# Optimization experiments

Hardware: AMD Instinct MI355X
Metric: run time of the kernel (lower is better)

Reference implementation:

```python
import jax, jax.numpy as jnp
import numpy as np

B, T, C = 8, 4096, 1024


def setup_inputs() -> dict:
    key = jax.random.key(0)
    ks = jax.random.split(key, 5)
    scales = (jnp.arange(C, dtype=jnp.float32) / C).reshape(1, 1, C)
    return {
        "x": jax.random.normal(ks[0], (B, T, C), dtype=jnp.float32),
        "time_decay": scales,
        "time_first": scales,
        "time_mix_k": scales,
        "time_mix_v": scales,
        "time_mix_r": scales,
        "Wk": jax.random.normal(ks[1], (C, C), dtype=jnp.float32) / np.sqrt(C),
        "Wv": jax.random.normal(ks[2], (C, C), dtype=jnp.float32) / np.sqrt(C),
        "Wr": jax.random.normal(ks[3], (C, C), dtype=jnp.float32) / np.sqrt(C),
        "Wo": jax.random.normal(ks[4], (C, C), dtype=jnp.float32) / np.sqrt(C),
    }


def _wkv(w_decay, u_first, k, v):
    # w_decay, u_first: [C]; k, v: [B, T, C]
    w = -jnp.exp(w_decay)  # per original: w = -w.exp()
    u = u_first
    kt = jnp.transpose(k, (1, 0, 2))  # [T, B, C]
    vt = jnp.transpose(v, (1, 0, 2))
    a0 = jnp.zeros((k.shape[0], k.shape[2]), dtype=k.dtype)
    b0 = jnp.zeros_like(a0)
    p0 = jnp.full_like(a0, -1e38)  # running max exponent

    def step(carry, kv):
        a, b, p = carry
        k_t, v_t = kv
        # output at t (includes bonus u for current token)
        q = jnp.maximum(p, u + k_t)
        e1 = jnp.exp(p - q)
        e2 = jnp.exp(u + k_t - q)
        y = (e1 * a + e2 * v_t) / (e1 * b + e2)
        # state update with decay w
        q2 = jnp.maximum(p + w, k_t)
        f1 = jnp.exp(p + w - q2)
        f2 = jnp.exp(k_t - q2)
        return (f1 * a + f2 * v_t, f1 * b + f2, q2), y

    _, y = jax.lax.scan(step, (a0, b0, p0), (kt, vt))
    return jnp.transpose(y, (1, 0, 2))  # [B, T, C]


def reference(x, time_decay, time_first, time_mix_k, time_mix_v, time_mix_r, Wk, Wv, Wr, Wo):
    # time shift: prev token, zero-padded at t=0 (ZeroPad2d((0,0,1,-1)))
    x_prev = jnp.pad(x, ((0, 0), (1, 0), (0, 0)))[:, :-1]
    # torch.lerp(a, b, w) = a + w*(b-a)
    xk = x_prev + time_mix_k * (x - x_prev)
    xv = x_prev + time_mix_v * (x - x_prev)
    xr = x_prev + time_mix_r * (x - x_prev)
    k = jnp.einsum('btc,dc->btd', xk, Wk)
    v = jnp.einsum('btc,dc->btd', xv, Wv)
    sr = jax.nn.sigmoid(jnp.einsum('btc,dc->btd', xr, Wr))
    wkv = _wkv(time_decay.reshape(-1), time_first.reshape(-1), k, v)
    return jnp.einsum('btc,dc->btd', sr * wkv, Wo)
```

## Files before the change

### kernel.cpp

```cpp
#include <hip/hip_runtime.h>
#include <hip/hip_bf16.h>
#include <hip/hip_fp16.h>


#define BH 8
#define TT 4096
#define CC 1024
#define NCH 64
#define CHL (TT / NCH)

typedef _Float16       f16x8  __attribute__((ext_vector_type(8)));
typedef float          f32x4  __attribute__((ext_vector_type(4)));
typedef unsigned short ushort_t;

__device__ __forceinline__ ushort_t f2h_u(float f) {
  return __half_as_ushort(__float2half(f));
}

#define GLOAD_LDS16(g, l)                                                     \
  __builtin_amdgcn_global_load_lds(                                           \
      (const __attribute__((address_space(1))) unsigned int*)(g),             \
      (__attribute__((address_space(3))) unsigned int*)(l), 16, 0, 0)

#define BARRIER() do { asm volatile("" ::: "memory");                        \
                       __builtin_amdgcn_s_barrier();                          \
                       asm volatile("" ::: "memory"); } while (0)

#define WAITALL() do { asm volatile("s_waitcnt vmcnt(0) lgkmcnt(0)" ::: "memory"); \
                       __builtin_amdgcn_sched_barrier(0); } while (0)

#define WAITV(n) do { asm volatile("s_waitcnt vmcnt(" #n ")" ::: "memory");  \
                      __builtin_amdgcn_sched_barrier(0); } while (0)

__global__ __launch_bounds__(256)
void split_w(const float* __restrict__ W0, const float* __restrict__ W1,
             const float* __restrict__ W2, const float* __restrict__ W3,
             ushort_t* __restrict__ out)
{
  int idx = blockIdx.x * 256 + threadIdx.x;
  int w = idx >> 20;
  int e = idx & (CC * CC - 1);
  const float* src = (w == 0) ? W0 : (w == 1) ? W1 : (w == 2) ? W2 : W3;
  out[(size_t)w * CC * CC + e] = f2h_u(src[e]);
}

__global__ __launch_bounds__(256)
void lerp3(const float* __restrict__ x,
           const float* __restrict__ mk, const float* __restrict__ mv,
           const float* __restrict__ mr,
           ushort_t* __restrict__ xk, ushort_t* __restrict__ xv,
           ushort_t* __restrict__ xr)
{
  const int idx = blockIdx.x * 256 + threadIdx.x;
  const int m = idx >> 8;
  const int c = (idx & 255) * 4;
  const size_t e = (size_t)m * CC + c;
  float4 cu = *(const float4*)(x + e);
  float4 pv = make_float4(0.f, 0.f, 0.f, 0.f);
  if ((m & (TT - 1)) != 0) pv = *(const float4*)(x + e - CC);

  const float* mixes[3] = {mk, mv, mr};
  ushort_t* outs[3] = {xk, xv, xr};
  #pragma unroll
  for (int z = 0; z < 3; ++z) {
    float4 mx = *(const float4*)(mixes[z] + c);
    float a0 = pv.x + mx.x * (cu.x - pv.x);
    float a1 = pv.y + mx.y * (cu.y - pv.y);
    float a2 = pv.z + mx.z * (cu.z - pv.z);
    float a3 = pv.w + mx.w * (cu.w - pv.w);
    *(ushort4*)(outs[z] + e) = make_ushort4(f2h_u(a0), f2h_u(a1), f2h_u(a2), f2h_u(a3));
  }
}

template<int EPI>
__global__ __launch_bounds__(512, 4)
void gemm_f16(const ushort_t* __restrict__ Ab, const ushort_t* __restrict__ Bb,
              void* __restrict__ Dv)
{
  constexpr int NS = 32;
  const size_t nbt = (size_t)BH * TT * CC;

  __shared__ __align__(16) ushort_t lds[2][12288];

  const int tid  = threadIdx.x;
  const int wave = tid >> 6, lane = tid & 63;
  const int wm = wave & 1, wn = wave >> 1;
  const int lr = lane & 15, kg = lane >> 4;

  const int z = blockIdx.z;
  const ushort_t* Ah = Ab + (size_t)z * nbt;
  const ushort_t* Bh = Bb + (size_t)z * CC * CC;

  const int bid = blockIdx.x;
  const int swz = (bid & 7) * 128 + (bid >> 3);
  const int m0 = (swz >> 2) * 128;
  const int n0 = (swz & 3) * 256;

  f32x4 acc[4][4] = {};

  auto stage = [&](int s) {
    if (s >= NS) return;
    const int kk = s * 32;
    {
      const int row = tid >> 2;
      const int q   = (tid & 3) ^ ((row >> 1) & 3);
      const ushort_t* src = Ah + (size_t)(m0 + row) * CC + kk + q * 8;
      ushort_t* dst = &lds[s & 1][0] + wave * 512;
      GLOAD_LDS16(src, dst);
    }
    #pragma unroll
    for (int c = 0; c < 2; ++c) {
      const int row = c * 128 + (tid >> 2);
      const int q   = (tid & 3) ^ ((row >> 1) & 3);
      const ushort_t* src = Bh + (size_t)(n0 + row) * CC + kk + q * 8;
      ushort_t* dst = &lds[s & 1][4096] + c * 4096 + wave * 512;
      GLOAD_LDS16(src, dst);
    }
  };
  auto rdA = [&](int b, int fm) -> f16x8 {
    const int row = wm * 64 + fm * 16 + lr;
    const int q   = kg ^ ((row >> 1) & 3);
    return *(const f16x8*)&lds[b][row * 32 + q * 8];
  };
  auto rdB = [&](int b, int fn) -> f16x8 {
    const int row = wn * 64 + fn * 16 + lr;
    const int q   = kg ^ ((row >> 1) & 3);
    return *(const f16x8*)&lds[b][4096 + row * 32 + q * 8];
  };

  stage(0); stage(1);
  WAITV(3);
  BARRIER();

  for (int s = 0; s < NS; ++s) {
    const int b = s & 1;

    f16x8 Bfr[4];
    #pragma unroll
    for (int fn = 0; fn < 4; ++fn) Bfr[fn] = rdB(b, fn);
    f16x8 Afr[4];
    #pragma unroll
    for (int fm = 0; fm < 4; ++fm) Afr[fm] = rdA(b, fm);

    __builtin_amdgcn_s_setprio(1);
    #pragma unroll
    for (int fm = 0; fm < 4; ++fm)
      #pragma unroll
      for (int fn = 0; fn < 4; ++fn)
        acc[fm][fn] = __builtin_amdgcn_mfma_f32_16x16x32_f16(Afr[fm], Bfr[fn], acc[fm][fn], 0, 0, 0);
    __builtin_amdgcn_s_setprio(0);

    WAITALL();
    BARRIER();
    stage(s + 2);
  }

  if (EPI == 0) {
    float* Df = (float*)Dv;
    #pragma unroll
    for (int fm = 0; fm < 4; ++fm)
      #pragma unroll
      for (int fn = 0; fn < 4; ++fn) {
        const int col  = n0 + wn * 64 + fn * 16 + lr;
        const int rowb = m0 + wm * 64 + fm * 16 + kg * 4;
        #pragma unroll
        for (int r = 0; r < 4; ++r)
          Df[(size_t)(rowb + r) * CC + col] = acc[fm][fn][r];
      }
  } else {
    __half* Dh = (__half*)Dv + (size_t)z * nbt;
    __half* ep = (__half*)&lds[0][0];
    const int rowl = tid >> 4;
    const int ck   = tid & 15;
    #pragma unroll
    for (int s = 0; s < 4; ++s) {
      __syncthreads();
      #pragma unroll
      for (int fn = 0; fn < 4; ++fn)
        #pragma unroll
        for (int r = 0; r < 4; ++r)
          ep[(wm * 16 + kg * 4 + r) * 280 + wn * 64 + fn * 16 + lr] =
              __float2half(acc[s][fn][r]);
      __syncthreads();
      uint4 v0 = *(const uint4*)&ep[rowl * 280 + ck * 16];
      uint4 v1 = *(const uint4*)&ep[rowl * 280 + ck * 16 + 8];
      const int grow = m0 + (rowl >> 4) * 64 + s * 16 + (rowl & 15);
      __half* dst = Dh + (size_t)grow * CC + n0 + ck * 16;
      *(uint4*)dst = v0;
      *(uint4*)(dst + 8) = v1;
    }
  }
}

__global__ __launch_bounds__(256)
void wkv_phase_a(const __half* __restrict__ kb, const __half* __restrict__ vb,
                 const float* __restrict__ decay,
                 float* __restrict__ SA, float* __restrict__ SB, float* __restrict__ SP)
{
  const int idx = blockIdx.x * 256 + threadIdx.x;
  const int c  = idx & (CC - 1);
  const int bc = idx >> 10;
  const int ch = bc & (NCH - 1);
  const int b  = bc >> 6;
  const float w = -__expf(decay[c]);
  float aa = 0.f, bb = 0.f, pp = -1e38f;
  size_t base = ((size_t)b * TT + (size_t)ch * CHL) * CC + c;
  #pragma unroll 4
  for (int t = 0; t < CHL; ++t) {
    const float kt = __half2float(kb[base]);
    const float vt = __half2float(vb[base]);
    const float q2 = fmaxf(pp + w, kt);
    const float f1 = __expf(pp + w - q2);
    const float f2 = __expf(kt - q2);
    aa = f1 * aa + f2 * vt; bb = f1 * bb + f2; pp = q2;
    base += CC;
  }
  SA[idx] = aa; SB[idx] = bb; SP[idx] = pp;
}

__global__ __launch_bounds__(256)
void wkv_combine(float* __restrict__ SA, float* __restrict__ SB, float* __restrict__ SP,
                 const float* __restrict__ decay)
{
  const int idx = blockIdx.x * 256 + threadIdx.x;
  const int c = idx & (CC - 1);
  const int b = idx >> 10;
  const float w  = -__expf(decay[c]);
  const float wL = w * (float)CHL;
  float aa = 0.f, bb = 0.f, pp = -1e38f;
  for (int ch = 0; ch < NCH; ++ch) {
    const size_t s = ((size_t)b * NCH + ch) * CC + c;
    const float la = SA[s], lb = SB[s], lp = SP[s];
    SA[s] = aa; SB[s] = bb; SP[s] = pp;
    const float pw = pp + wL;
    const float q  = fmaxf(pw, lp);
    const float e1 = __expf(pw - q);
    const float e2 = __expf(lp - q);
    aa = e1 * aa + e2 * la; bb = e1 * bb + e2 * lb; pp = q;
  }
}

__global__ __launch_bounds__(256)
void wkv_phase_c(const __half* __restrict__ kb, const __half* __restrict__ vb,
                 const __half* __restrict__ rb, const float* __restrict__ decay,
                 const float* __restrict__ first,
                 const float* __restrict__ SA, const float* __restrict__ SB,
                 const float* __restrict__ SP,
                 ushort_t* __restrict__ yh)
{
  const int idx = blockIdx.x * 256 + threadIdx.x;
  const int c  = idx & (CC - 1);
  const int bc = idx >> 10;
  const int ch = bc & (NCH - 1);
  const int b  = bc >> 6;
  const float w = -__expf(decay[c]);
  const float u = first[c];
  float aa = SA[idx], bb = SB[idx], pp = SP[idx];
  size_t base = ((size_t)b * TT + (size_t)ch * CHL) * CC + c;
  #pragma unroll 4
  for (int t = 0; t < CHL; ++t) {
    const float kt = __half2float(kb[base]);
    const float vt = __half2float(vb[base]);
    const float rt = __half2float(rb[base]);
    const float q  = fmaxf(pp, u + kt);
    const float e1 = __expf(pp - q);
    const float e2 = __expf(u + kt - q);
    const float yv = (e1 * aa + e2 * vt) / (e1 * bb + e2);
    const float sr = 1.f / (1.f + __expf(-rt));
    yh[base] = f2h_u(sr * yv);
    const float q2 = fmaxf(pp + w, kt);
    const float f1 = __expf(pp + w - q2);
    const float f2 = __expf(kt - q2);
    aa = f1 * aa + f2 * vt; bb = f1 * bb + f2; pp = q2;
    base += CC;
  }
}

extern "C" void kernel_launch(void* const* d_in, const int* in_sizes, int n_in,
                              void* d_out, int out_size, void* d_ws, size_t ws_size,
                              hipStream_t stream) {
  const float* x     = (const float*)d_in[0];
  const float* decay = (const float*)d_in[1];
  const float* first = (const float*)d_in[2];
  const float* mk    = (const float*)d_in[3];
  const float* mv    = (const float*)d_in[4];
  const float* mr    = (const float*)d_in[5];
  const float* Wk    = (const float*)d_in[6];
  const float* Wv    = (const float*)d_in[7];
  const float* Wr    = (const float*)d_in[8];
  const float* Wo    = (const float*)d_in[9];
  float* out = (float*)d_out;

  const size_t nbt = (size_t)BH * TT * CC;
  const size_t WS  = (size_t)CC * CC;
  char* p = (char*)d_ws;
  ushort_t* xk   = (ushort_t*)(p);
  ushort_t* xv   = (ushort_t*)(p +  67108864);
  ushort_t* xr   = (ushort_t*)(p + 134217728);
  __half*   kbuf = (__half*)  (p + 201326592);
  __half*   vbuf = (__half*)  (p + 268435456);
  __half*   rbuf = (__half*)  (p + 335544320);
  ushort_t* Wsp  = (ushort_t*)(p + 402653184);
  float*    SA   = (float*)   (p + 411041792);
  float*    SB   = (float*)   (p + 413138944);
  float*    SP   = (float*)   (p + 415236096);

  dim3 blk(256);
  const dim3 gblk(512);
  const unsigned lerpg = (unsigned)(nbt / 4 / 256);

  split_w<<<dim3(4 * CC * CC / 256), blk, 0, stream>>>(Wk, Wv, Wr, Wo, Wsp);
  lerp3<<<dim3(lerpg), blk, 0, stream>>>(x, mk, mv, mr, xk, xv, xr);

  gemm_f16<1><<<dim3(1024, 1, 3), gblk, 0, stream>>>(xk, Wsp, (void*)kbuf);

  const int nscan = BH * NCH * CC;
  wkv_phase_a<<<dim3(nscan / 256), blk, 0, stream>>>(kbuf, vbuf, decay, SA, SB, SP);
  wkv_combine<<<dim3(BH * CC / 256), blk, 0, stream>>>(SA, SB, SP, decay);
  wkv_phase_c<<<dim3(nscan / 256), blk, 0, stream>>>(kbuf, vbuf, rbuf, decay, first,
                                                     SA, SB, SP, xk);

  gemm_f16<0><<<dim3(1024, 1, 1), gblk, 0, stream>>>(xk, Wsp + 3 * WS, (void*)out);
}
```

Before: 517.4 us.

## Shrink GEMM tiles to 128x128 and load B fragments directly from global

```diff
diff --git a/kernel.cpp b/kernel.cpp
--- a/kernel.cpp
+++ b/kernel.cpp
@@ -73,14 +73,15 @@
 }
 
 template<int EPI>
-__global__ __launch_bounds__(512, 4)
+__global__ __launch_bounds__(256, 3)
 void gemm_f16(const ushort_t* __restrict__ Ab, const ushort_t* __restrict__ Bb,
               void* __restrict__ Dv)
 {
   constexpr int NS = 32;
   const size_t nbt = (size_t)BH * TT * CC;
 
-  __shared__ __align__(16) ushort_t lds[2][12288];
+  __shared__ __align__(16) ushort_t lds[2][4096];
+  __shared__ __align__(16) __half  ep[32 * 136];
 
   const int tid  = threadIdx.x;
   const int wave = tid >> 6, lane = tid & 63;
@@ -92,28 +93,22 @@
   const ushort_t* Bh = Bb + (size_t)z * CC * CC;
 
   const int bid = blockIdx.x;
-  const int swz = (bid & 7) * 128 + (bid >> 3);
-  const int m0 = (swz >> 2) * 128;
-  const int n0 = (swz & 3) * 256;
+  const int swz = (bid & 7) * 256 + (bid >> 3);
+  const int m0 = (swz >> 3) * 128;
+  const int n0 = (swz & 7) * 128;
 
   f32x4 acc[4][4] = {};
 
   auto stage = [&](int s) {
     if (s >= NS) return;
     const int kk = s * 32;
-    {
-      const int row = tid >> 2;
-      const int q   = (tid & 3) ^ ((row >> 1) & 3);
-      const ushort_t* src = Ah + (size_t)(m0 + row) * CC + kk + q * 8;
-      ushort_t* dst = &lds[s & 1][0] + wave * 512;
-      GLOAD_LDS16(src, dst);
-    }
     #pragma unroll
     for (int c = 0; c < 2; ++c) {
-      const int row = c * 128 + (tid >> 2);
-      const int q   = (tid & 3) ^ ((row >> 1) & 3);
-      const ushort_t* src = Bh + (size_t)(n0 + row) * CC + kk + q * 8;
-      ushort_t* dst = &lds[s & 1][4096] + c * 4096 + wave * 512;
+      const int slot = c * 256 + tid;
+      const int row  = slot >> 2;
+      const int q    = (slot & 3) ^ ((row >> 1) & 3);
+      const ushort_t* src = Ah + (size_t)(m0 + row) * CC + kk + q * 8;
+      ushort_t* dst = &lds[s & 1][0] + c * 2048 + wave * 512;
       GLOAD_LDS16(src, dst);
     }
   };
@@ -122,37 +117,59 @@
     const int q   = kg ^ ((row >> 1) & 3);
     return *(const f16x8*)&lds[b][row * 32 + q * 8];
   };
-  auto rdB = [&](int b, int fn) -> f16x8 {
-    const int row = wn * 64 + fn * 16 + lr;
-    const int q   = kg ^ ((row >> 1) & 3);
-    return *(const f16x8*)&lds[b][4096 + row * 32 + q * 8];
+  auto ldB = [&](int s, f16x8* Bf) {
+    const int kk = s * 32 + kg * 8;
+    #pragma unroll
+    for (int fn = 0; fn < 4; ++fn) {
+      const int row = n0 + wn * 64 + fn * 16 + lr;
+      Bf[fn] = *(const f16x8*)(Bh + (size_t)row * CC + kk);
+    }
   };
 
-  stage(0); stage(1);
-  WAITV(3);
+  f16x8 B0[4], B1[4];
+
+  stage(0);
+  ldB(0, B0);
+  stage(1);
+  WAITV(2);
   BARRIER();
 
-  for (int s = 0; s < NS; ++s) {
-    const int b = s & 1;
-
-    f16x8 Bfr[4];
-    #pragma unroll
-    for (int fn = 0; fn < 4; ++fn) Bfr[fn] = rdB(b, fn);
-    f16x8 Afr[4];
-    #pragma unroll
-    for (int fm = 0; fm < 4; ++fm) Afr[fm] = rdA(b, fm);
-
-    __builtin_amdgcn_s_setprio(1);
-    #pragma unroll
-    for (int fm = 0; fm < 4; ++fm)
-      #pragma unroll
-      for (int fn = 0; fn < 4; ++fn)
-        acc[fm][fn] = __builtin_amdgcn_mfma_f32_16x16x32_f16(Afr[fm], Bfr[fn], acc[fm][fn], 0, 0, 0);
-    __builtin_amdgcn_s_setprio(0);
-
-    WAITALL();
-    BARRIER();
-    stage(s + 2);
+  #pragma unroll 1
+  for (int t = 0; t < NS / 2; ++t) {
+    {
+      const int s = 2 * t;
+      f16x8 Afr[4];
+      #pragma unroll
+      for (int fm = 0; fm < 4; ++fm) Afr[fm] = rdA(0, fm);
+      ldB(s + 1, B1);
+      __builtin_amdgcn_s_setprio(1);
+      #pragma unroll
+      for (int fm = 0; fm < 4; ++fm)
+        #pragma unroll
+        for (int fn = 0; fn < 4; ++fn)
+          acc[fm][fn] = __builtin_amdgcn_mfma_f32_16x16x32_f16(Afr[fm], B0[fn], acc[fm][fn], 0, 0, 0);
+      __builtin_amdgcn_s_setprio(0);
+      WAITALL();
+      BARRIER();
+      stage(s + 2);
+    }
+    {
+      const int s = 2 * t + 1;
+      f16x8 Afr[4];
+      #pragma unroll
+      for (int fm = 0; fm < 4; ++fm) Afr[fm] = rdA(1, fm);
+      if (s + 1 < NS) ldB(s + 1, B0);
+      __builtin_amdgcn_s_setprio(1);
+      #pragma unroll
+      for (int fm = 0; fm < 4; ++fm)
+        #pragma unroll
+        for (int fn = 0; fn < 4; ++fn)
+          acc[fm][fn] = __builtin_amdgcn_mfma_f32_16x16x32_f16(Afr[fm], B1[fn], acc[fm][fn], 0, 0, 0);
+      __builtin_amdgcn_s_setprio(0);
+      WAITALL();
+      BARRIER();
+      stage(s + 2);
+    }
   }
 
   if (EPI == 0) {
@@ -169,9 +186,8 @@
       }
   } else {
     __half* Dh = (__half*)Dv + (size_t)z * nbt;
-    __half* ep = (__half*)&lds[0][0];
-    const int rowl = tid >> 4;
-    const int ck   = tid & 15;
+    const int rowl = tid >> 3;
+    const int ck   = tid & 7;
     #pragma unroll
     for (int s = 0; s < 4; ++s) {
       __syncthreads();
@@ -179,11 +195,11 @@
       for (int fn = 0; fn < 4; ++fn)
         #pragma unroll
         for (int r = 0; r < 4; ++r)
-          ep[(wm * 16 + kg * 4 + r) * 280 + wn * 64 + fn * 16 + lr] =
+          ep[(wm * 16 + kg * 4 + r) * 136 + wn * 64 + fn * 16 + lr] =
               __float2half(acc[s][fn][r]);
       __syncthreads();
-      uint4 v0 = *(const uint4*)&ep[rowl * 280 + ck * 16];
-      uint4 v1 = *(const uint4*)&ep[rowl * 280 + ck * 16 + 8];
+      uint4 v0 = *(const uint4*)&ep[rowl * 136 + ck * 16];
+      uint4 v1 = *(const uint4*)&ep[rowl * 136 + ck * 16 + 8];
       const int grow = m0 + (rowl >> 4) * 64 + s * 16 + (rowl & 15);
       __half* dst = Dh + (size_t)grow * CC + n0 + ck * 16;
       *(uint4*)dst = v0;
@@ -306,13 +322,12 @@
   float*    SP   = (float*)   (p + 415236096);
 
   dim3 blk(256);
-  const dim3 gblk(512);
   const unsigned lerpg = (unsigned)(nbt / 4 / 256);
 
   split_w<<<dim3(4 * CC * CC / 256), blk, 0, stream>>>(Wk, Wv, Wr, Wo, Wsp);
   lerp3<<<dim3(lerpg), blk, 0, stream>>>(x, mk, mv, mr, xk, xv, xr);
 
-  gemm_f16<1><<<dim3(1024, 1, 3), gblk, 0, stream>>>(xk, Wsp, (void*)kbuf);
+  gemm_f16<1><<<dim3(2048, 1, 3), blk, 0, stream>>>(xk, Wsp, (void*)kbuf);
 
   const int nscan = BH * NCH * CC;
   wkv_phase_a<<<dim3(nscan / 256), blk, 0, stream>>>(kbuf, vbuf, decay, SA, SB, SP);
@@ -320,5 +335,5 @@
   wkv_phase_c<<<dim3(nscan / 256), blk, 0, stream>>>(kbuf, vbuf, rbuf, decay, first,
                                                      SA, SB, SP, xk);
 
-  gemm_f16<0><<<dim3(1024, 1, 1), gblk, 0, stream>>>(xk, Wsp + 3 * WS, (void*)out);
-}
+  gemm_f16<0><<<dim3(2048, 1, 1), blk, 0, stream>>>(xk, Wsp + 3 * WS, (void*)out);
+}
```

Result: slower. 778.3 us (+50.4%).
